# Kernel tuning notes

Hardware: AMD Instinct MI355X
Metric: run time of the kernel (lower is better)

Reference implementation:

```python
import jax, jax.numpy as jnp
import numpy as np

GRID_SIZE = 10
DEGREE = 3


def bspline_basis(x, grid_size=GRID_SIZE, degree=DEGREE):
    """Cox-de Boor B-spline basis on a uniform grid over [-1, 1].
    x: (...,) -> (..., grid_size + degree)
    """
    h = 2.0 / grid_size
    # extended knot vector, length grid_size + 2*degree + 1
    knots = jnp.arange(-degree, grid_size + degree + 1, dtype=x.dtype) * h - 1.0
    # keep inputs inside the grid support (standard KAN practice)
    x = jnp.clip(x, -1.0, 1.0 - 1e-6)
    xe = x[..., None]
    b = ((xe >= knots[:-1]) & (xe < knots[1:])).astype(x.dtype)  # degree-0, (..., K-1)
    for d in range(1, degree + 1):
        left = (xe - knots[: -(d + 1)]) / (knots[d:-1] - knots[: -(d + 1)]) * b[..., :-1]
        right = (knots[d + 1:] - xe) / (knots[d + 1:] - knots[1:-d]) * b[..., 1:]
        b = left + right
    return b  # (..., grid_size + degree)


def setup_inputs() -> dict:
    key = jax.random.key(0)
    k1, k2, k3 = jax.random.split(key, 3)
    B, S, IN, OUT, E = 4, 2048, 256, 256, 8
    n_basis = GRID_SIZE + DEGREE
    x = jax.random.normal(k1, (B, S, IN), dtype=jnp.float32)
    coeff = jax.random.normal(k2, (E, n_basis), dtype=jnp.float32) * 0.1
    gating_weights = jax.random.normal(k3, (IN, OUT, E), dtype=jnp.float32)
    return {"x": x, "coeff": coeff, "gating_weights": gating_weights}


def reference(x, coeff, gating_weights):
    # spline experts: elementwise basis eval, then per-expert linear combo
    basis = bspline_basis(x)                              # (B, S, I, n_basis)
    expert_outputs = jnp.einsum('bsin,en->bsie', basis, coeff)  # (B, S, I, E)
    gates = jax.nn.softmax(gating_weights, axis=-1)       # (I, O, E)
    out = jnp.einsum('bsie,ioe->bso', expert_outputs, gates)
    return out
```

## Files before the change

### kernel.cpp

```cpp
#include <hip/hip_runtime.h>

typedef __attribute__((ext_vector_type(8))) short short8;
typedef __attribute__((ext_vector_type(4))) float f32x4;

#define IN_DIM 256
#define OUT_DIM 256
#define NB 16
#define KDIM (IN_DIM * NB)
#define TM 32
#define TN 128
#define BK 64
#define KSPLIT 2
#define IPER (IN_DIM / KSPLIT)
#define STEPS (IPER / 4)
#define ABUF (TM * BK * 2)
#define BBUF (TN * BK * 2)

__device__ __forceinline__ unsigned short f2bf(float f) {
  union { float f; unsigned int u; } v; v.f = f;
  unsigned int r = v.u + 0x7fffu + ((v.u >> 16) & 1u);
  return (unsigned short)(r >> 16);
}

__device__ __forceinline__ void glds16(const void* g, void* l) {
  __builtin_amdgcn_global_load_lds((__attribute__((address_space(1))) const void*)g,
                                   (__attribute__((address_space(3))) void*)l, 16, 0, 0);
}

__device__ __forceinline__ void spline_row(float xv, unsigned* d) {
  float xc = fminf(fmaxf(xv, -1.0f), 1.0f - 1e-6f);
  float u = (xc + 1.0f) * 5.0f;
  int c = (int)u;
  c = c > 9 ? 9 : (c < 0 ? 0 : c);
  float tt = u - (float)c;
  float omt = 1.0f - tt;
  float t2 = tt * tt, t3 = t2 * tt;
  float b0 = omt * omt * omt * (1.0f / 6.0f);
  float b1 = (3.0f * t3 - 6.0f * t2 + 4.0f) * (1.0f / 6.0f);
  float b2 = (-3.0f * t3 + 3.0f * t2 + 3.0f * tt + 1.0f) * (1.0f / 6.0f);
  float b3 = t3 * (1.0f / 6.0f);
  unsigned h0 = f2bf(b0), h1 = f2bf(b1), h2 = f2bf(b2), h3 = f2bf(b3);
  const int a = c >> 1;
  const bool odd = (c & 1) != 0;
  unsigned p01 = h0 | (h1 << 16);
  unsigned p23 = h2 | (h3 << 16);
  unsigned A0 = odd ? (h0 << 16) : p01;
  unsigned A1 = odd ? (h1 | (h2 << 16)) : p23;
  unsigned A2 = odd ? h3 : 0u;
#pragma unroll
  for (int j = 0; j < 8; ++j) {
    unsigned v = (j == a) ? A0 : 0u;
    v = (j == a + 1) ? A1 : v;
    v = (j == a + 2) ? A2 : v;
    d[j] = v;
  }
}

__global__ __launch_bounds__(256) void kan_prep(const float* __restrict__ coeff,
                                                const float* __restrict__ gw,
                                                unsigned short* __restrict__ BmT,
                                                float* __restrict__ out) {
  __shared__ float csh[104];
  __shared__ unsigned short tile[16][256];
  const int t = threadIdx.x;
  {
    const int bid = blockIdx.y * 16 + blockIdx.x;
    float4 z; z.x = z.y = z.z = z.w = 0.f;
    float4* ob = (float4*)out;
#pragma unroll
    for (int j = 0; j < 8; ++j) ob[(size_t)bid * 2048 + j * 256 + t] = z;
  }
  if (t < 104) csh[t] = coeff[t];
  __syncthreads();
  const int otile = blockIdx.x, itile = blockIdx.y;
  const int il = t >> 4, ol = t & 15;
  const int i = itile * 16 + il;
  const int o = otile * 16 + ol;
  const float* g = gw + (size_t)(i * OUT_DIM + o) * 8;
  float4 g0 = *(const float4*)g;
  float4 g1 = *(const float4*)(g + 4);
  float ge[8] = {g0.x, g0.y, g0.z, g0.w, g1.x, g1.y, g1.z, g1.w};
  float mx = ge[0];
#pragma unroll
  for (int e = 1; e < 8; ++e) mx = fmaxf(mx, ge[e]);
  float p[8]; float s = 0.f;
#pragma unroll
  for (int e = 0; e < 8; ++e) { p[e] = __expf(ge[e] - mx); s += p[e]; }
  const float inv = 1.0f / s;
  unsigned short row[16];
#pragma unroll
  for (int n = 0; n < 13; ++n) {
    float w = 0.f;
#pragma unroll
    for (int e = 0; e < 8; ++e) w += p[e] * csh[e * 13 + n];
    row[n] = f2bf(w * inv);
  }
  row[13] = 0; row[14] = 0; row[15] = 0;
  int4* dst = (int4*)&tile[ol][il * 16];
  dst[0] = *(const int4*)&row[0];
  dst[1] = *(const int4*)&row[8];
  __syncthreads();
  const int oo = t >> 4, ck = t & 15;
  int4 v0 = *(const int4*)&tile[oo][ck * 16];
  int4 v1 = *(const int4*)&tile[oo][ck * 16 + 8];
  int4* out4 = (int4*)(BmT + (size_t)(otile * 16 + oo) * KDIM + itile * 256 + ck * 16);
  out4[0] = v0;
  out4[1] = v1;
}

__global__ __launch_bounds__(256, 4) void kan_gemm(const float* __restrict__ x,
                                                   const unsigned short* __restrict__ BmT,
                                                   float* __restrict__ out) {
  __shared__ unsigned short Ash[2][TM * BK];
  __shared__ unsigned short Bsh[2][TN * BK];

  const int t = threadIdx.x;
  const int lane = t & 63;
  const int wave = t >> 6;
  const int wn = wave;
  const int mb = blockIdx.x * TM;
  const int ob = blockIdx.y * TN;
  const int i0 = blockIdx.z * IPER;

  const int r = t & 31;
  const int il = (t >> 5) & 3;
  const bool astage = t < 128;
  const float* xptr = x + (size_t)(mb + r) * IN_DIM + i0 + il;
  char* const abase = (char*)&Ash[0][0] + r * 128;
  const int msw = r & 7;
  const int aw0 = ((2 * il + 0) ^ msw) << 4;
  const int aw1 = ((2 * il + 1) ^ msw) << 4;

  const unsigned short* bgbase =
      BmT + (size_t)(ob + (t >> 3)) * KDIM + i0 * NB + ((t & 7) ^ ((t >> 3) & 7)) * 8;
  char* const bl = (char*)&Bsh[0][0] + wave * 1024;

  f32x4 acc[2][2];
#pragma unroll
  for (int a = 0; a < 2; ++a)
#pragma unroll
    for (int b = 0; b < 2; ++b) acc[a][b] = (f32x4){0.f, 0.f, 0.f, 0.f};

  int aoff[2], boff[2];
#pragma unroll
  for (int f = 0; f < 2; ++f) {
    const int ro = f * 16 + (lane & 15);
    aoff[f] = ro * 128 + (((lane >> 4) ^ (ro & 7)) << 4);
    const int bo = wn * 32 + f * 16 + (lane & 15);
    boff[f] = bo * 128 + (((lane >> 4) ^ (bo & 7)) << 4);
  }

  {
#pragma unroll
    for (int q = 0; q < 4; ++q)
      glds16(bgbase + (size_t)q * 32 * KDIM, bl + q * 4096);
    if (astage) {
      float xv = *xptr;
      unsigned d[8];
      spline_row(xv, d);
      *(int4*)(abase + aw0) = *(const int4*)&d[0];
      *(int4*)(abase + aw1) = *(const int4*)&d[4];
    }
    asm volatile("s_waitcnt vmcnt(0)" ::: "memory");
  }

  for (int s = 0; s < STEPS; ++s) {
    __syncthreads();
    const int cur = s & 1;
    float xn = 0.f;
    if (s + 1 < STEPS) {
      if (astage) xn = xptr[(s + 1) * 4];
#pragma unroll
      for (int q = 0; q < 4; ++q)
        glds16(bgbase + (size_t)(s + 1) * BK + (size_t)q * 32 * KDIM,
               bl + (1 - cur) * BBUF + q * 4096);
    }
    const char* Ac = (const char*)&Ash[0][0] + cur * ABUF;
    const char* Bc = (const char*)&Bsh[0][0] + cur * BBUF;
    __builtin_amdgcn_s_setprio(1);
#pragma unroll
    for (int kc = 0; kc < 2; ++kc) {
      short8 af[2], bfr[2];
#pragma unroll
      for (int f = 0; f < 2; ++f) af[f] = *(const short8*)(Ac + (aoff[f] ^ (kc << 6)));
#pragma unroll
      for (int f = 0; f < 2; ++f) bfr[f] = *(const short8*)(Bc + (boff[f] ^ (kc << 6)));
#pragma unroll
      for (int mf = 0; mf < 2; ++mf)
#pragma unroll
        for (int nf = 0; nf < 2; ++nf)
          acc[mf][nf] = __builtin_amdgcn_mfma_f32_16x16x32_bf16(af[mf], bfr[nf], acc[mf][nf], 0, 0, 0);
    }
    __builtin_amdgcn_s_setprio(0);
    if (astage && s + 1 < STEPS) {
      unsigned d[8];
      spline_row(xn, d);
      char* an = abase + (1 - cur) * ABUF;
      *(int4*)(an + aw0) = *(const int4*)&d[0];
      *(int4*)(an + aw1) = *(const int4*)&d[4];
    }
  }

#pragma unroll
  for (int mf = 0; mf < 2; ++mf)
#pragma unroll
    for (int nf = 0; nf < 2; ++nf)
#pragma unroll
      for (int q = 0; q < 4; ++q) {
        int row = mb + mf * 16 + ((lane >> 4) << 2) + q;
        int col = ob + wn * 32 + nf * 16 + (lane & 15);
        atomicAdd(out + (size_t)row * OUT_DIM + col, acc[mf][nf][q]);
      }
}

extern "C" void kernel_launch(void* const* d_in, const int* in_sizes, int n_in,
                              void* d_out, int out_size, void* d_ws, size_t ws_size,
                              hipStream_t stream) {
  const float* x     = (const float*)d_in[0];
  const float* coeff = (const float*)d_in[1];
  const float* gw    = (const float*)d_in[2];
  float* out = (float*)d_out;
  unsigned short* BmT = (unsigned short*)d_ws;

  kan_prep<<<dim3(16, 16), dim3(256), 0, stream>>>(coeff, gw, BmT, out);
  dim3 grid(8192 / TM, OUT_DIM / TN, KSPLIT);
  kan_gemm<<<grid, dim3(256), 0, stream>>>(x, BmT, out);
}
```

Measured before the change: 110.2 us.

## Drop split-K atomics and deepen the pipeline with triple-buffered async B and x loads

Removes the K-split, so each block covers the full 256-input reduction. Its results are written with plain stores, which drops the output zeroing in the prep kernel and the atomic adds. The B tile becomes triple-buffered and x values are now staged into shared memory with async global-to-LDS loads two to three steps ahead. Each step synchronises with a partial vmcnt wait plus a raw barrier instead of waiting for all loads to finish. In exchange the grid has half as many blocks, each block uses more LDS, and launch bounds drop to 2 blocks per SIMD, which may reduce occupancy and parallelism.

```diff
diff --git a/kernel.cpp b/kernel.cpp
--- a/kernel.cpp
+++ b/kernel.cpp
@@ -10,11 +10,9 @@
 #define TM 32
 #define TN 128
 #define BK 64
-#define KSPLIT 2
-#define IPER (IN_DIM / KSPLIT)
-#define STEPS (IPER / 4)
-#define ABUF (TM * BK * 2)
-#define BBUF (TN * BK * 2)
+#define STEPS 64
+#define ABUF 4096
+#define BTILE 16384
 
 __device__ __forceinline__ unsigned short f2bf(float f) {
   union { float f; unsigned int u; } v; v.f = f;
@@ -58,18 +56,10 @@
 
 __global__ __launch_bounds__(256) void kan_prep(const float* __restrict__ coeff,
                                                 const float* __restrict__ gw,
-                                                unsigned short* __restrict__ BmT,
-                                                float* __restrict__ out) {
+                                                unsigned short* __restrict__ BmT) {
   __shared__ float csh[104];
   __shared__ unsigned short tile[16][256];
   const int t = threadIdx.x;
-  {
-    const int bid = blockIdx.y * 16 + blockIdx.x;
-    float4 z; z.x = z.y = z.z = z.w = 0.f;
-    float4* ob = (float4*)out;
-#pragma unroll
-    for (int j = 0; j < 8; ++j) ob[(size_t)bid * 2048 + j * 256 + t] = z;
-  }
   if (t < 104) csh[t] = coeff[t];
   __syncthreads();
   const int otile = blockIdx.x, itile = blockIdx.y;
@@ -108,11 +98,12 @@
   out4[1] = v1;
 }
 
-__global__ __launch_bounds__(256, 4) void kan_gemm(const float* __restrict__ x,
+__global__ __launch_bounds__(256, 2) void kan_gemm(const float* __restrict__ x,
                                                    const unsigned short* __restrict__ BmT,
                                                    float* __restrict__ out) {
   __shared__ unsigned short Ash[2][TM * BK];
-  __shared__ unsigned short Bsh[2][TN * BK];
+  __shared__ unsigned short Bsh[3][TN * BK];
+  __shared__ float Xsh[3 * 256];
 
   const int t = threadIdx.x;
   const int lane = t & 63;
@@ -120,20 +111,19 @@
   const int wn = wave;
   const int mb = blockIdx.x * TM;
   const int ob = blockIdx.y * TN;
-  const int i0 = blockIdx.z * IPER;
 
   const int r = t & 31;
   const int il = (t >> 5) & 3;
   const bool astage = t < 128;
-  const float* xptr = x + (size_t)(mb + r) * IN_DIM + i0 + il;
   char* const abase = (char*)&Ash[0][0] + r * 128;
   const int msw = r & 7;
   const int aw0 = ((2 * il + 0) ^ msw) << 4;
   const int aw1 = ((2 * il + 1) ^ msw) << 4;
 
+  const float* const xg = x + (size_t)(mb + (lane & 31)) * IN_DIM;
+
   const unsigned short* bgbase =
-      BmT + (size_t)(ob + (t >> 3)) * KDIM + i0 * NB + ((t & 7) ^ ((t >> 3) & 7)) * 8;
-  char* const bl = (char*)&Bsh[0][0] + wave * 1024;
+      BmT + (size_t)(ob + (t >> 3)) * KDIM + ((t & 7) ^ ((t >> 3) & 7)) * 8;
 
   f32x4 acc[2][2];
 #pragma unroll
@@ -151,55 +141,72 @@
   }
 
   {
+    float x0v = 0.f;
+    if (astage) x0v = x[(size_t)(mb + r) * IN_DIM + il];
 #pragma unroll
     for (int q = 0; q < 4; ++q)
-      glds16(bgbase + (size_t)q * 32 * KDIM, bl + q * 4096);
+      glds16(bgbase + (size_t)q * 32 * KDIM,
+             (char*)&Bsh[0][0] + wave * 1024 + q * 4096);
+    glds16(xg + 4, (char*)Xsh + 1 * 1024);
+#pragma unroll
+    for (int q = 0; q < 4; ++q)
+      glds16(bgbase + (size_t)BK + (size_t)q * 32 * KDIM,
+             (char*)&Bsh[0][0] + BTILE + wave * 1024 + q * 4096);
+    glds16(xg + 8, (char*)Xsh + 2 * 1024);
     if (astage) {
-      float xv = *xptr;
+      unsigned d[8];
+      spline_row(x0v, d);
+      *(int4*)(abase + aw0) = *(const int4*)&d[0];
+      *(int4*)(abase + aw1) = *(const int4*)&d[4];
+    }
+    asm volatile("s_waitcnt vmcnt(5) lgkmcnt(0)" ::: "memory");
+    __builtin_amdgcn_sched_barrier(0);
+    __builtin_amdgcn_s_barrier();
+  }
+
+  for (int s = 0; s < STEPS; ++s) {
+    const int cur = s & 1;
+    {
+      const int tf = (s + 2 < STEPS) ? s + 2 : STEPS - 1;
+      char* bd = (char*)&Bsh[0][0] + ((s + 2) % 3) * BTILE + wave * 1024;
+#pragma unroll
+      for (int q = 0; q < 4; ++q)
+        glds16(bgbase + (size_t)tf * BK + (size_t)q * 32 * KDIM, bd + q * 4096);
+    }
+    {
+      const int xf = (s + 3 < STEPS) ? s + 3 : STEPS - 1;
+      glds16(xg + 4 * xf, (char*)Xsh + ((s + 3) % 3) * 1024);
+    }
+    const char* Ac = (const char*)&Ash[0][0] + cur * ABUF;
+    const char* Bc = (const char*)&Bsh[0][0] + (s % 3) * BTILE;
+    __builtin_amdgcn_s_setprio(1);
+#pragma unroll
+    for (int kc = 0; kc < 2; ++kc) {
+      short8 af[2], bfr[2];
+#pragma unroll
+      for (int f = 0; f < 2; ++f) af[f] = *(const short8*)(Ac + (aoff[f] ^ (kc << 6)));
+#pragma unroll
+      for (int f = 0; f < 2; ++f) bfr[f] = *(const short8*)(Bc + (boff[f] ^ (kc << 6)));
+#pragma unroll
+      for (int mf = 0; mf < 2; ++mf)
+#pragma unroll
+        for (int nf = 0; nf < 2; ++nf)
+          acc[mf][nf] = __builtin_amdgcn_mfma_f32_16x16x32_bf16(af[mf], bfr[nf], acc[mf][nf], 0, 0, 0);
+    }
+    __builtin_amdgcn_s_setprio(0);
+    if (astage && s + 1 < STEPS) {
+      float xv = Xsh[((s + 1) % 3) * 256 + 4 * r + il];
       unsigned d[8];
       spline_row(xv, d);
-      *(int4*)(abase + aw0) = *(const int4*)&d[0];
-      *(int4*)(abase + aw1) = *(const int4*)&d[4];
-    }
-    asm volatile("s_waitcnt vmcnt(0)" ::: "memory");
-  }
-
-  for (int s = 0; s < STEPS; ++s) {
-    __syncthreads();
-    const int cur = s & 1;
-    float xn = 0.f;
-    if (s + 1 < STEPS) {
-      if (astage) xn = xptr[(s + 1) * 4];
-#pragma unroll
-      for (int q = 0; q < 4; ++q)
-        glds16(bgbase + (size_t)(s + 1) * BK + (size_t)q * 32 * KDIM,
-               bl + (1 - cur) * BBUF + q * 4096);
-    }
-    const char* Ac = (const char*)&Ash[0][0] + cur * ABUF;
-    const char* Bc = (const char*)&Bsh[0][0] + cur * BBUF;
-    __builtin_amdgcn_s_setprio(1);
-#pragma unroll
-    for (int kc = 0; kc < 2; ++kc) {
-      short8 af[2], bfr[2];
-#pragma unroll
-      for (int f = 0; f < 2; ++f) af[f] = *(const short8*)(Ac + (aoff[f] ^ (kc << 6)));
-#pragma unroll
-      for (int f = 0; f < 2; ++f) bfr[f] = *(const short8*)(Bc + (boff[f] ^ (kc << 6)));
-#pragma unroll
-      for (int mf = 0; mf < 2; ++mf)
-#pragma unroll
-        for (int nf = 0; nf < 2; ++nf)
-          acc[mf][nf] = __builtin_amdgcn_mfma_f32_16x16x32_bf16(af[mf], bfr[nf], acc[mf][nf], 0, 0, 0);
-    }
-    __builtin_amdgcn_s_setprio(0);
-    if (astage && s + 1 < STEPS) {
-      unsigned d[8];
-      spline_row(xn, d);
       char* an = abase + (1 - cur) * ABUF;
       *(int4*)(an + aw0) = *(const int4*)&d[0];
       *(int4*)(an + aw1) = *(const int4*)&d[4];
     }
-  }
+    asm volatile("s_waitcnt vmcnt(5) lgkmcnt(0)" ::: "memory");
+    __builtin_amdgcn_sched_barrier(0);
+    __builtin_amdgcn_s_barrier();
+  }
+  asm volatile("s_waitcnt vmcnt(0) lgkmcnt(0)" ::: "memory");
 
 #pragma unroll
   for (int mf = 0; mf < 2; ++mf)
@@ -209,7 +216,7 @@
       for (int q = 0; q < 4; ++q) {
         int row = mb + mf * 16 + ((lane >> 4) << 2) + q;
         int col = ob + wn * 32 + nf * 16 + (lane & 15);
-        atomicAdd(out + (size_t)row * OUT_DIM + col, acc[mf][nf][q]);
+        out[(size_t)row * OUT_DIM + col] = acc[mf][nf][q];
       }
 }
 
@@ -222,7 +229,7 @@
   float* out = (float*)d_out;
   unsigned short* BmT = (unsigned short*)d_ws;
 
-  kan_prep<<<dim3(16, 16), dim3(256), 0, stream>>>(coeff, gw, BmT, out);
-  dim3 grid(8192 / TM, OUT_DIM / TN, KSPLIT);
+  kan_prep<<<dim3(16, 16), dim3(256), 0, stream>>>(coeff, gw, BmT);
+  dim3 grid(8192 / TM, OUT_DIM / TN);
   kan_gemm<<<grid, dim3(256), 0, stream>>>(x, BmT, out);
 }
```

Result: slower. 126.9 us (+15.1%).
